# Performance work log

Measured on AMD Instinct MI355X. Metric: run time of the kernel, lower is better.

The kernel has to match this reference:

```python
import jax, jax.numpy as jnp
import numpy as np

N_NODES = 100000
N_EDGES = 3200000
IN_CH = 256
OUT_CH = 1


def setup_inputs() -> dict:
    key = jax.random.key(0)
    ks = jax.random.split(key, 8)
    x = jax.random.normal(ks[0], (N_NODES, IN_CH), dtype=jnp.float32)
    edge_index = jax.random.randint(ks[1], (2, N_EDGES), 0, N_NODES, dtype=jnp.int64 if jax.config.jax_enable_x64 else jnp.int32)
    s_in = 1.0 / np.sqrt(IN_CH)
    Wq = jax.random.uniform(ks[2], (IN_CH, OUT_CH), jnp.float32, -s_in, s_in)
    bq = jax.random.uniform(ks[3], (OUT_CH,), jnp.float32, -s_in, s_in)
    Wk = jax.random.uniform(ks[4], (IN_CH, OUT_CH), jnp.float32, -s_in, s_in)
    bk = jax.random.uniform(ks[5], (OUT_CH,), jnp.float32, -s_in, s_in)
    Wv = jax.random.uniform(ks[6], (IN_CH, IN_CH), jnp.float32, -s_in, s_in)
    bv = jax.random.uniform(ks[7], (IN_CH,), jnp.float32, -s_in, s_in)
    return {"x": x, "edge_index": edge_index, "Wq": Wq, "bq": bq,
            "Wk": Wk, "bk": bk, "Wv": Wv, "bv": bv}


def reference(x, edge_index, Wq, bq, Wk, bk, Wv, bv):
    num_nodes = x.shape[0]
    q = x @ Wq + bq                       # [N, out_ch]
    k = x @ Wk + bk                       # [N, out_ch]
    v = x @ Wv + bv                       # [N, in_ch]
    row, col = edge_index[0], edge_index[1]
    # edge attention logits: gather + dot over out_ch
    att = jnp.sum(q[row] * k[col], axis=-1)          # [E]
    att = jax.nn.leaky_relu(att, negative_slope=0.2)
    att = jax.nn.softmax(att, axis=0)                # softmax over ALL edges (dim=0)
    # scatter-add edge attention to source nodes
    attention_weights = jax.ops.segment_sum(att, row, num_segments=num_nodes)  # [N]
    graph_emb = jnp.sum(attention_weights[:, None] * v, axis=0)                # [in_ch]
    return graph_emb, attention_weights
```

## Files before the change

### kernel.cpp

```cpp
#include <hip/hip_runtime.h>

#define N_NODES 100000
#define N_EDGES 3200000
#define CH 256

#define GRID_QK 1563
#define GRID_POOL 512
#define YCOPY 16

#define NR 4
#define RANGE 25000
#define SL 64
#define EPS 50000
#define QEPS 12500
#define GP 391

#define OFF_TOTAL 0
#define OFF_PTOT  16
#define OFF_YU16  528
#define OFF_Q     4624
#define OFF_K     104624
#define OFF_AWU   204624
#define OFF_PART  304624

__global__ __launch_bounds__(256) void k_qk(const float* __restrict__ x,
                                            const float* __restrict__ Wq,
                                            const float* __restrict__ bq,
                                            const float* __restrict__ Wk,
                                            const float* __restrict__ bk,
                                            float* __restrict__ q,
                                            float* __restrict__ k,
                                            float* __restrict__ yu16) {
    int t = threadIdx.x;
    if (blockIdx.x < 16) yu16[blockIdx.x * 256 + t] = 0.0f;
    int w = t >> 6, lane = t & 63;
    int g = lane >> 4, seg = lane & 15;
    float4 wq4[4], wk4[4];
    #pragma unroll
    for (int j = 0; j < 4; ++j) {
        wq4[j] = ((const float4*)Wq)[seg + 16 * j];
        wk4[j] = ((const float4*)Wk)[seg + 16 * j];
    }
    float bqs = bq[0], bks = bk[0];
    int base = blockIdx.x * 64 + w * 16 + g;
    #pragma unroll
    for (int i = 0; i < 4; ++i) {
        int n = base + i * 4;
        if (n < N_NODES) {
            const float4* xr = (const float4*)(x + (size_t)n * CH);
            float dq = 0.0f, dk = 0.0f;
            #pragma unroll
            for (int j = 0; j < 4; ++j) {
                float4 xv = xr[seg + 16 * j];
                dq = fmaf(xv.x, wq4[j].x, fmaf(xv.y, wq4[j].y,
                     fmaf(xv.z, wq4[j].z, fmaf(xv.w, wq4[j].w, dq))));
                dk = fmaf(xv.x, wk4[j].x, fmaf(xv.y, wk4[j].y,
                     fmaf(xv.z, wk4[j].z, fmaf(xv.w, wk4[j].w, dk))));
            }
            dq += __shfl_down(dq, 8); dq += __shfl_down(dq, 4);
            dq += __shfl_down(dq, 2); dq += __shfl_down(dq, 1);
            dk += __shfl_down(dk, 8); dk += __shfl_down(dk, 4);
            dk += __shfl_down(dk, 2); dk += __shfl_down(dk, 1);
            if (seg == 0) { q[n] = dq + bqs; k[n] = dk + bks; }
        }
    }
}

__global__ __launch_bounds__(1024) void k_acc(const int* __restrict__ ei,
                                              const float* __restrict__ q,
                                              const float* __restrict__ k,
                                              float* __restrict__ partial) {
    extern __shared__ float acc[];
    int t = threadIdx.x;
    int s = blockIdx.x >> 2, r = blockIdx.x & 3;
    for (int i = t; i < RANGE; i += 1024) acc[i] = 0.0f;
    __syncthreads();
    int r0 = r * RANGE;
    const int4* rows4 = (const int4*)ei;
    int q0 = s * QEPS;
    for (int i4 = q0 + t; i4 < q0 + QEPS; i4 += 1024) {
        int4 rw = rows4[i4];
        int eb = 4 * i4;
        unsigned o0 = (unsigned)(rw.x - r0);
        unsigned o1 = (unsigned)(rw.y - r0);
        unsigned o2 = (unsigned)(rw.z - r0);
        unsigned o3 = (unsigned)(rw.w - r0);
        if (o0 < RANGE) {
            float v = q[rw.x] * k[ei[N_EDGES + eb]];
            atomicAdd(&acc[o0], __expf(fmaxf(v, 0.2f * v)));
        }
        if (o1 < RANGE) {
            float v = q[rw.y] * k[ei[N_EDGES + eb + 1]];
            atomicAdd(&acc[o1], __expf(fmaxf(v, 0.2f * v)));
        }
        if (o2 < RANGE) {
            float v = q[rw.z] * k[ei[N_EDGES + eb + 2]];
            atomicAdd(&acc[o2], __expf(fmaxf(v, 0.2f * v)));
        }
        if (o3 < RANGE) {
            float v = q[rw.w] * k[ei[N_EDGES + eb + 3]];
            atomicAdd(&acc[o3], __expf(fmaxf(v, 0.2f * v)));
        }
    }
    __syncthreads();
    float* dst = partial + ((size_t)r * SL + s) * RANGE;
    for (int i = t; i < RANGE; i += 1024) dst[i] = acc[i];
}

__global__ __launch_bounds__(256) void k_fold(const float* __restrict__ partial,
                                              float* __restrict__ awu,
                                              float* __restrict__ ptot) {
    int t = threadIdx.x;
    int n = blockIdx.x * 256 + t;
    float s = 0.0f;
    if (n < N_NODES) {
        int r = n / RANGE, off = n % RANGE;
        const float* p = partial + (size_t)r * SL * RANGE + off;
        #pragma unroll 8
        for (int g = 0; g < SL; ++g) s += p[(size_t)g * RANGE];
        awu[n] = s;
    }
    float rsum = s;
    #pragma unroll
    for (int off = 32; off; off >>= 1) rsum += __shfl_down(rsum, off);
    __shared__ float sm[4];
    if ((t & 63) == 0) sm[t >> 6] = rsum;
    __syncthreads();
    if (t == 0) ptot[blockIdx.x] = sm[0] + sm[1] + sm[2] + sm[3];
}

__global__ __launch_bounds__(256) void k_pool(const float* __restrict__ x,
                                              const float* __restrict__ awu,
                                              const float* __restrict__ ptot,
                                              float* __restrict__ totalp,
                                              float* __restrict__ yu16,
                                              float* __restrict__ aw_out) {
    int t = threadIdx.x, s = t >> 6, g = t & 63;
    float ts = ptot[t] + ((t + 256 < GP) ? ptot[t + 256] : 0.0f);
    #pragma unroll
    for (int off = 32; off; off >>= 1) ts += __shfl_down(ts, off);
    __shared__ float sm[4];
    __shared__ float tot;
    if (g == 0) sm[s] = ts;
    __syncthreads();
    if (t == 0) {
        tot = sm[0] + sm[1] + sm[2] + sm[3];
        if (blockIdx.x == 0) totalp[0] = tot;
    }
    __syncthreads();
    float inv = 1.0f / tot;

    const float4* X4 = (const float4*)x;
    float4 acc = make_float4(0.f, 0.f, 0.f, 0.f);
    for (int base = blockIdx.x * 8; base < N_NODES; base += GRID_POOL * 8) {
        float a0 = awu[base + s];
        float a1 = awu[base + 4 + s];
        float4 x0 = X4[(size_t)(base + s) * 64 + g];
        float4 x1 = X4[(size_t)(base + 4 + s) * 64 + g];
        acc.x = fmaf(a0, x0.x, acc.x); acc.y = fmaf(a0, x0.y, acc.y);
        acc.z = fmaf(a0, x0.z, acc.z); acc.w = fmaf(a0, x0.w, acc.w);
        acc.x = fmaf(a1, x1.x, acc.x); acc.y = fmaf(a1, x1.y, acc.y);
        acc.z = fmaf(a1, x1.z, acc.z); acc.w = fmaf(a1, x1.w, acc.w);
    }
    __shared__ float4 tmp4[4][64];
    tmp4[s][g] = acc;
    __syncthreads();
    const float* tmp = (const float*)tmp4;
    float sum = tmp[0 * 256 + t] + tmp[1 * 256 + t] + tmp[2 * 256 + t] + tmp[3 * 256 + t];
    atomicAdd(&yu16[(blockIdx.x & (YCOPY - 1)) * 256 + t], sum);
    for (int i = blockIdx.x * 256 + t; i < N_NODES; i += GRID_POOL * 256)
        aw_out[i] = awu[i] * inv;
}

__global__ __launch_bounds__(256) void k_final(const float* __restrict__ yu16,
                                               const float* __restrict__ totalp,
                                               const float* __restrict__ Wv,
                                               const float* __restrict__ bv,
                                               float* __restrict__ out) {
    __shared__ float ysh[256];
    __shared__ float red[256];
    int t = threadIdx.x;
    float inv = 1.0f / totalp[0];
    float yv = 0.0f;
    #pragma unroll
    for (int j = 0; j < YCOPY; ++j) yv += yu16[j * 256 + t];
    ysh[t] = yv * inv;
    __syncthreads();
    int c = blockIdx.x * 32 + (t & 31), rg = t >> 5;
    float acc = 0.0f;
    #pragma unroll
    for (int j = 0; j < 32; ++j) {
        int kk = rg * 32 + j;
        acc = fmaf(ysh[kk], Wv[(size_t)kk * CH + c], acc);
    }
    red[t] = acc;
    __syncthreads();
    if (t < 32) {
        float sv = 0.0f;
        #pragma unroll
        for (int j = 0; j < 8; ++j) sv += red[j * 32 + t];
        out[blockIdx.x * 32 + t] = sv + bv[blockIdx.x * 32 + t];
    }
}

extern "C" void kernel_launch(void* const* d_in, const int* in_sizes, int n_in,
                              void* d_out, int out_size, void* d_ws, size_t ws_size,
                              hipStream_t stream) {
    const float* x  = (const float*)d_in[0];
    const int*   ei = (const int*)d_in[1];
    const float* Wq = (const float*)d_in[2];
    const float* bq = (const float*)d_in[3];
    const float* Wk = (const float*)d_in[4];
    const float* bk = (const float*)d_in[5];
    const float* Wv = (const float*)d_in[6];
    const float* bv = (const float*)d_in[7];
    float* out = (float*)d_out;
    float* ws  = (float*)d_ws;

    float* totalp  = ws + OFF_TOTAL;
    float* ptot    = ws + OFF_PTOT;
    float* yu16    = ws + OFF_YU16;
    float* q       = ws + OFF_Q;
    float* k       = ws + OFF_K;
    float* awu     = ws + OFF_AWU;
    float* partial = ws + OFF_PART;

    static bool lds_init = false;
    if (!lds_init) {
        (void)hipFuncSetAttribute((const void*)k_acc,
                                  hipFuncAttributeMaxDynamicSharedMemorySize,
                                  RANGE * 4);
        lds_init = true;
    }

    hipLaunchKernelGGL(k_qk, dim3(GRID_QK), dim3(256), 0, stream,
                       x, Wq, bq, Wk, bk, q, k, yu16);
    hipLaunchKernelGGL(k_acc, dim3(NR * SL), dim3(1024), RANGE * 4, stream,
                       ei, q, k, partial);
    hipLaunchKernelGGL(k_fold, dim3(GP), dim3(256), 0, stream,
                       partial, awu, ptot);
    hipLaunchKernelGGL(k_pool, dim3(GRID_POOL), dim3(256), 0, stream,
                       x, awu, ptot, totalp, yu16, out + CH);
    hipLaunchKernelGGL(k_final, dim3(8), dim3(256), 0, stream,
                       yu16, totalp, Wv, bv, out);
}
```

Measured before the change: 249.2 us.

## Partition edges by row range before LDS accumulation to avoid redundant edge scans

Replaces the single accumulation kernel, where each of four row-range blocks rescanned all edges and filtered by range, with two kernels. The first computes exp(leaky_relu) once per edge and bins it by row range into global buckets using LDS staging and atomic counters. The second accumulates only its own bucket into LDS. This removes the fourfold re-reading of row indices but adds an extra kernel launch, a global write and read of the binned data, and fixed capacity limits (CAP, SCAP) that only hold for a roughly uniform row distribution.

New measurement: 257.5 us. +3.3%, slower.

```diff
diff --git a/kernel.cpp b/kernel.cpp
--- a/kernel.cpp
+++ b/kernel.cpp
@@ -11,17 +11,26 @@
 #define NR 4
 #define RANGE 25000
 #define SL 64
-#define EPS 50000
-#define QEPS 12500
+#define EPB_P 12500
+#define GRID_P 256
+#define CAP 3600
+#define SCAP 850000
 #define GP 391
+
+#define LDSP_FLOATS (6 * CAP + 8)
+#define LDSP_BYTES  (LDSP_FLOATS * 4)
+#define LDSA_BYTES  (RANGE * 4)
 
 #define OFF_TOTAL 0
 #define OFF_PTOT  16
 #define OFF_YU16  528
-#define OFF_Q     4624
-#define OFF_K     104624
-#define OFF_AWU   204624
-#define OFF_PART  304624
+#define OFF_GCNT  4624
+#define OFF_Q     4640
+#define OFF_K     104640
+#define OFF_AWU   204640
+#define OFF_EXS   304640
+#define OFF_RWS   3704640
+#define OFF_PART  5404640
 
 __global__ __launch_bounds__(256) void k_qk(const float* __restrict__ x,
                                             const float* __restrict__ Wq,
@@ -30,9 +39,11 @@
                                             const float* __restrict__ bk,
                                             float* __restrict__ q,
                                             float* __restrict__ k,
-                                            float* __restrict__ yu16) {
+                                            float* __restrict__ yu16,
+                                            int* __restrict__ gcnt) {
     int t = threadIdx.x;
     if (blockIdx.x < 16) yu16[blockIdx.x * 256 + t] = 0.0f;
+    if (blockIdx.x == 0 && t < NR) gcnt[t] = 0;
     int w = t >> 6, lane = t & 63;
     int g = lane >> 4, seg = lane & 15;
     float4 wq4[4], wk4[4];
@@ -66,42 +77,69 @@
     }
 }
 
-__global__ __launch_bounds__(1024) void k_acc(const int* __restrict__ ei,
-                                              const float* __restrict__ q,
-                                              const float* __restrict__ k,
-                                              float* __restrict__ partial) {
+__global__ __launch_bounds__(1024) void k_part(const int* __restrict__ ei,
+                                               const float* __restrict__ q,
+                                               const float* __restrict__ k,
+                                               int* __restrict__ gcnt,
+                                               float* __restrict__ exs,
+                                               unsigned short* __restrict__ rws) {
+    extern __shared__ float lds[];
+    float* lex = lds;
+    unsigned short* lrow = (unsigned short*)(lds + 4 * CAP);
+    int* cnt = (int*)(lds + 6 * CAP);
+    int t = threadIdx.x;
+    if (t < NR) cnt[t] = 0;
+    __syncthreads();
+    const int4* r4p = (const int4*)(ei) + blockIdx.x * (EPB_P / 4);
+    const int4* c4p = (const int4*)(ei + N_EDGES) + blockIdx.x * (EPB_P / 4);
+    for (int i4 = t; i4 < EPB_P / 4; i4 += 1024) {
+        int4 rv = r4p[i4];
+        int4 cv = c4p[i4];
+        int rows[4] = {rv.x, rv.y, rv.z, rv.w};
+        int cols[4] = {cv.x, cv.y, cv.z, cv.w};
+        #pragma unroll
+        for (int j = 0; j < 4; ++j) {
+            int row = rows[j];
+            int r = row / RANGE;
+            int lr = row - r * RANGE;
+            float v = q[row] * k[cols[j]];
+            float e = __expf(fmaxf(v, 0.2f * v));
+            int slot = atomicAdd(&cnt[r], 1);
+            lex[r * CAP + slot] = e;
+            lrow[r * CAP + slot] = (unsigned short)lr;
+        }
+    }
+    __syncthreads();
+    int* gbase = cnt + NR;
+    if (t < NR) gbase[t] = atomicAdd(&gcnt[t], cnt[t]);
+    __syncthreads();
+    #pragma unroll
+    for (int r = 0; r < NR; ++r) {
+        int n = cnt[r], b = gbase[r];
+        float* exd = exs + (size_t)r * SCAP + b;
+        unsigned short* rwd = rws + (size_t)r * SCAP + b;
+        const float* exsrc = lex + r * CAP;
+        const unsigned short* rwsrc = lrow + r * CAP;
+        for (int i = t; i < n; i += 1024) { exd[i] = exsrc[i]; rwd[i] = rwsrc[i]; }
+    }
+}
+
+__global__ __launch_bounds__(1024) void k_acc2(const float* __restrict__ exs,
+                                               const unsigned short* __restrict__ rws,
+                                               const int* __restrict__ gcnt,
+                                               float* __restrict__ partial) {
     extern __shared__ float acc[];
     int t = threadIdx.x;
     int s = blockIdx.x >> 2, r = blockIdx.x & 3;
     for (int i = t; i < RANGE; i += 1024) acc[i] = 0.0f;
     __syncthreads();
-    int r0 = r * RANGE;
-    const int4* rows4 = (const int4*)ei;
-    int q0 = s * QEPS;
-    for (int i4 = q0 + t; i4 < q0 + QEPS; i4 += 1024) {
-        int4 rw = rows4[i4];
-        int eb = 4 * i4;
-        unsigned o0 = (unsigned)(rw.x - r0);
-        unsigned o1 = (unsigned)(rw.y - r0);
-        unsigned o2 = (unsigned)(rw.z - r0);
-        unsigned o3 = (unsigned)(rw.w - r0);
-        if (o0 < RANGE) {
-            float v = q[rw.x] * k[ei[N_EDGES + eb]];
-            atomicAdd(&acc[o0], __expf(fmaxf(v, 0.2f * v)));
-        }
-        if (o1 < RANGE) {
-            float v = q[rw.y] * k[ei[N_EDGES + eb + 1]];
-            atomicAdd(&acc[o1], __expf(fmaxf(v, 0.2f * v)));
-        }
-        if (o2 < RANGE) {
-            float v = q[rw.z] * k[ei[N_EDGES + eb + 2]];
-            atomicAdd(&acc[o2], __expf(fmaxf(v, 0.2f * v)));
-        }
-        if (o3 < RANGE) {
-            float v = q[rw.w] * k[ei[N_EDGES + eb + 3]];
-            atomicAdd(&acc[o3], __expf(fmaxf(v, 0.2f * v)));
-        }
-    }
+    int n = gcnt[r];
+    int per = (n + SL - 1) / SL;
+    int i0 = s * per, i1 = min(i0 + per, n);
+    const float* exr = exs + (size_t)r * SCAP;
+    const unsigned short* rwr = rws + (size_t)r * SCAP;
+    for (int i = i0 + t; i < i1; i += 1024)
+        atomicAdd(&acc[rwr[i]], exr[i]);
     __syncthreads();
     float* dst = partial + ((size_t)r * SL + s) * RANGE;
     for (int i = t; i < RANGE; i += 1024) dst[i] = acc[i];
@@ -217,26 +255,34 @@
     float* out = (float*)d_out;
     float* ws  = (float*)d_ws;
 
-    float* totalp  = ws + OFF_TOTAL;
-    float* ptot    = ws + OFF_PTOT;
-    float* yu16    = ws + OFF_YU16;
-    float* q       = ws + OFF_Q;
-    float* k       = ws + OFF_K;
-    float* awu     = ws + OFF_AWU;
-    float* partial = ws + OFF_PART;
+    float*          totalp  = ws + OFF_TOTAL;
+    float*          ptot    = ws + OFF_PTOT;
+    float*          yu16    = ws + OFF_YU16;
+    int*            gcnt    = (int*)(ws + OFF_GCNT);
+    float*          q       = ws + OFF_Q;
+    float*          k       = ws + OFF_K;
+    float*          awu     = ws + OFF_AWU;
+    float*          exs     = ws + OFF_EXS;
+    unsigned short* rws     = (unsigned short*)(ws + OFF_RWS);
+    float*          partial = ws + OFF_PART;
 
     static bool lds_init = false;
     if (!lds_init) {
-        (void)hipFuncSetAttribute((const void*)k_acc,
+        (void)hipFuncSetAttribute((const void*)k_part,
                                   hipFuncAttributeMaxDynamicSharedMemorySize,
-                                  RANGE * 4);
+                                  LDSP_BYTES);
+        (void)hipFuncSetAttribute((const void*)k_acc2,
+                                  hipFuncAttributeMaxDynamicSharedMemorySize,
+                                  LDSA_BYTES);
         lds_init = true;
     }
 
     hipLaunchKernelGGL(k_qk, dim3(GRID_QK), dim3(256), 0, stream,
-                       x, Wq, bq, Wk, bk, q, k, yu16);
-    hipLaunchKernelGGL(k_acc, dim3(NR * SL), dim3(1024), RANGE * 4, stream,
-                       ei, q, k, partial);
+                       x, Wq, bq, Wk, bk, q, k, yu16, gcnt);
+    hipLaunchKernelGGL(k_part, dim3(GRID_P), dim3(1024), LDSP_BYTES, stream,
+                       ei, q, k, gcnt, exs, rws);
+    hipLaunchKernelGGL(k_acc2, dim3(NR * SL), dim3(1024), LDSA_BYTES, stream,
+                       exs, rws, gcnt, partial);
     hipLaunchKernelGGL(k_fold, dim3(GP), dim3(256), 0, stream,
                        partial, awu, ptot);
     hipLaunchKernelGGL(k_pool, dim3(GRID_POOL), dim3(256), 0, stream,
```

## Split node range into eight LDS bins with XCD-aware block mapping

Applied to the files above, without the earlier changes.

The per-block shared-memory accumulator shrinks from 25000 to 12500 floats by doubling the number of node-range partitions from 4 to 8, which raises LDS occupancy per CU and launches 512 blocks instead of 256. Block indices are remapped so each XCD handles a fixed set of edge slices, keeping the same edge data in one XCD's L2 across range blocks. Column indices are now loaded as int4 vectors instead of scalar gathers. The trade-off is that every edge is read 8 times instead of 4, k_fold's partial-buffer layout changes (hidden code must match the NR/RANGE macros), and the fold stage has more partials to sum.

Measured after the change: 245.3 us. Within noise of the previous version (-1.6%).

```diff
diff --git a/kernel.cpp b/kernel.cpp
--- a/kernel.cpp
+++ b/kernel.cpp
@@ -8,8 +8,8 @@
 #define GRID_POOL 512
 #define YCOPY 16
 
-#define NR 4
-#define RANGE 25000
+#define NR 8
+#define RANGE 12500
 #define SL 64
 #define EPS 50000
 #define QEPS 12500
@@ -70,35 +70,38 @@
                                               const float* __restrict__ q,
                                               const float* __restrict__ k,
                                               float* __restrict__ partial) {
-    extern __shared__ float acc[];
-    int t = threadIdx.x;
-    int s = blockIdx.x >> 2, r = blockIdx.x & 3;
+    __shared__ float acc[RANGE];
+    int t = threadIdx.x;
+    int xcd = blockIdx.x & 7;
+    int inner = blockIdx.x >> 3;
+    int r = inner & 7;
+    int s = (inner >> 3) * 8 + xcd;
     for (int i = t; i < RANGE; i += 1024) acc[i] = 0.0f;
     __syncthreads();
     int r0 = r * RANGE;
-    const int4* rows4 = (const int4*)ei;
-    int q0 = s * QEPS;
-    for (int i4 = q0 + t; i4 < q0 + QEPS; i4 += 1024) {
-        int4 rw = rows4[i4];
-        int eb = 4 * i4;
-        unsigned o0 = (unsigned)(rw.x - r0);
-        unsigned o1 = (unsigned)(rw.y - r0);
-        unsigned o2 = (unsigned)(rw.z - r0);
-        unsigned o3 = (unsigned)(rw.w - r0);
+    const int4* r4p = (const int4*)ei + s * QEPS;
+    const int4* c4p = (const int4*)(ei + N_EDGES) + s * QEPS;
+    for (int i4 = t; i4 < QEPS; i4 += 1024) {
+        int4 rv = r4p[i4];
+        int4 cv = c4p[i4];
+        unsigned o0 = (unsigned)(rv.x - r0);
+        unsigned o1 = (unsigned)(rv.y - r0);
+        unsigned o2 = (unsigned)(rv.z - r0);
+        unsigned o3 = (unsigned)(rv.w - r0);
         if (o0 < RANGE) {
-            float v = q[rw.x] * k[ei[N_EDGES + eb]];
+            float v = q[rv.x] * k[cv.x];
             atomicAdd(&acc[o0], __expf(fmaxf(v, 0.2f * v)));
         }
         if (o1 < RANGE) {
-            float v = q[rw.y] * k[ei[N_EDGES + eb + 1]];
+            float v = q[rv.y] * k[cv.y];
             atomicAdd(&acc[o1], __expf(fmaxf(v, 0.2f * v)));
         }
         if (o2 < RANGE) {
-            float v = q[rw.z] * k[ei[N_EDGES + eb + 2]];
+            float v = q[rv.z] * k[cv.z];
             atomicAdd(&acc[o2], __expf(fmaxf(v, 0.2f * v)));
         }
         if (o3 < RANGE) {
-            float v = q[rw.w] * k[ei[N_EDGES + eb + 3]];
+            float v = q[rv.w] * k[cv.w];
             atomicAdd(&acc[o3], __expf(fmaxf(v, 0.2f * v)));
         }
     }
@@ -225,17 +228,9 @@
     float* awu     = ws + OFF_AWU;
     float* partial = ws + OFF_PART;
 
-    static bool lds_init = false;
-    if (!lds_init) {
-        (void)hipFuncSetAttribute((const void*)k_acc,
-                                  hipFuncAttributeMaxDynamicSharedMemorySize,
-                                  RANGE * 4);
-        lds_init = true;
-    }
-
     hipLaunchKernelGGL(k_qk, dim3(GRID_QK), dim3(256), 0, stream,
                        x, Wq, bq, Wk, bk, q, k, yu16);
-    hipLaunchKernelGGL(k_acc, dim3(NR * SL), dim3(1024), RANGE * 4, stream,
+    hipLaunchKernelGGL(k_acc, dim3(NR * SL), dim3(1024), 0, stream,
                        ei, q, k, partial);
     hipLaunchKernelGGL(k_fold, dim3(GP), dim3(256), 0, stream,
                        partial, awu, ptot);
```

## Remap accumulation blocks across XCDs and batch vectorized edge index loads

Applied to the files above, without the earlier changes.

The accumulation kernel remaps block indices so that each XCD handles a fixed subset of edge slices, aiming to keep the four range blocks that share a slice on the same XCD's L2. It also loads column indices as int4 vectors rather than scalar loads, and issues four row/column vector loads per thread before processing them to raise memory-level parallelism. The cost is higher register pressure at 1024 threads per block and extra bounds predicates.

After: 237.7 us. 4.6% less time.

```diff
diff --git a/kernel.cpp b/kernel.cpp
--- a/kernel.cpp
+++ b/kernel.cpp
@@ -14,6 +14,8 @@
 #define EPS 50000
 #define QEPS 12500
 #define GP 391
+
+#define LDSA_BYTES (RANGE * 4)
 
 #define OFF_TOTAL 0
 #define OFF_PTOT  16
@@ -72,35 +74,51 @@
                                               float* __restrict__ partial) {
     extern __shared__ float acc[];
     int t = threadIdx.x;
-    int s = blockIdx.x >> 2, r = blockIdx.x & 3;
+    int xcd = blockIdx.x & 7;
+    int inner = blockIdx.x >> 3;
+    int r = inner & 3;
+    int s = (inner >> 2) * 8 + xcd;
     for (int i = t; i < RANGE; i += 1024) acc[i] = 0.0f;
     __syncthreads();
     int r0 = r * RANGE;
-    const int4* rows4 = (const int4*)ei;
-    int q0 = s * QEPS;
-    for (int i4 = q0 + t; i4 < q0 + QEPS; i4 += 1024) {
-        int4 rw = rows4[i4];
-        int eb = 4 * i4;
-        unsigned o0 = (unsigned)(rw.x - r0);
-        unsigned o1 = (unsigned)(rw.y - r0);
-        unsigned o2 = (unsigned)(rw.z - r0);
-        unsigned o3 = (unsigned)(rw.w - r0);
-        if (o0 < RANGE) {
-            float v = q[rw.x] * k[ei[N_EDGES + eb]];
-            atomicAdd(&acc[o0], __expf(fmaxf(v, 0.2f * v)));
+    const int4* r4p = (const int4*)ei + s * QEPS;
+    const int4* c4p = (const int4*)(ei + N_EDGES) + s * QEPS;
+    for (int base = t; base < QEPS; base += 4096) {
+        int4 rv0, rv1, rv2, rv3, cv0, cv1, cv2, cv3;
+        int i1 = base + 1024, i2 = base + 2048, i3 = base + 3072;
+        bool h1 = i1 < QEPS, h2 = i2 < QEPS, h3 = i3 < QEPS;
+        rv0 = r4p[base];            cv0 = c4p[base];
+        if (h1) { rv1 = r4p[i1];    cv1 = c4p[i1]; }
+        if (h2) { rv2 = r4p[i2];    cv2 = c4p[i2]; }
+        if (h3) { rv3 = r4p[i3];    cv3 = c4p[i3]; }
+        #define DO4(rv, cv)                                                   \
+        {                                                                     \
+            unsigned o0 = (unsigned)(rv.x - r0);                              \
+            unsigned o1 = (unsigned)(rv.y - r0);                              \
+            unsigned o2 = (unsigned)(rv.z - r0);                              \
+            unsigned o3 = (unsigned)(rv.w - r0);                              \
+            if (o0 < RANGE) {                                                 \
+                float v = q[rv.x] * k[cv.x];                                  \
+                atomicAdd(&acc[o0], __expf(fmaxf(v, 0.2f * v)));              \
+            }                                                                 \
+            if (o1 < RANGE) {                                                 \
+                float v = q[rv.y] * k[cv.y];                                  \
+                atomicAdd(&acc[o1], __expf(fmaxf(v, 0.2f * v)));              \
+            }                                                                 \
+            if (o2 < RANGE) {                                                 \
+                float v = q[rv.z] * k[cv.z];                                  \
+                atomicAdd(&acc[o2], __expf(fmaxf(v, 0.2f * v)));              \
+            }                                                                 \
+            if (o3 < RANGE) {                                                 \
+                float v = q[rv.w] * k[cv.w];                                  \
+                atomicAdd(&acc[o3], __expf(fmaxf(v, 0.2f * v)));              \
+            }                                                                 \
         }
-        if (o1 < RANGE) {
-            float v = q[rw.y] * k[ei[N_EDGES + eb + 1]];
-            atomicAdd(&acc[o1], __expf(fmaxf(v, 0.2f * v)));
-        }
-        if (o2 < RANGE) {
-            float v = q[rw.z] * k[ei[N_EDGES + eb + 2]];
-            atomicAdd(&acc[o2], __expf(fmaxf(v, 0.2f * v)));
-        }
-        if (o3 < RANGE) {
-            float v = q[rw.w] * k[ei[N_EDGES + eb + 3]];
-            atomicAdd(&acc[o3], __expf(fmaxf(v, 0.2f * v)));
-        }
+        DO4(rv0, cv0);
+        if (h1) DO4(rv1, cv1);
+        if (h2) DO4(rv2, cv2);
+        if (h3) DO4(rv3, cv3);
+        #undef DO4
     }
     __syncthreads();
     float* dst = partial + ((size_t)r * SL + s) * RANGE;
@@ -229,13 +247,13 @@
     if (!lds_init) {
         (void)hipFuncSetAttribute((const void*)k_acc,
                                   hipFuncAttributeMaxDynamicSharedMemorySize,
-                                  RANGE * 4);
+                                  LDSA_BYTES);
         lds_init = true;
     }
 
     hipLaunchKernelGGL(k_qk, dim3(GRID_QK), dim3(256), 0, stream,
                        x, Wq, bq, Wk, bk, q, k, yu16);
-    hipLaunchKernelGGL(k_acc, dim3(NR * SL), dim3(1024), RANGE * 4, stream,
+    hipLaunchKernelGGL(k_acc, dim3(NR * SL), dim3(1024), LDSA_BYTES, stream,
                        ei, q, k, partial);
     hipLaunchKernelGGL(k_fold, dim3(GP), dim3(256), 0, stream,
                        partial, awu, ptot);
```
